# Kernel optimization log

Measured on AMD Instinct MI355X. Metric: run time of the kernel, lower is better.

Reference implementation:

```python
import jax, jax.numpy as jnp
import numpy as np
from jax import lax

# Dense-equivalent of the spconv net: SubMConv/SparseConv with stride 1 and
# size-preserving padding on a dense input reduce to ordinary conv2d.
# Layer chain: (1->64,k1) PReLU (64->256,k3) PReLU (256->512,k3) PReLU
# (512->256,k3) PReLU (256->64,k3) PReLU (64->1,k3) PReLU, then symmetrize.

CHANS = [(1, 64, 1), (64, 256, 3), (256, 512, 3), (512, 256, 3), (256, 64, 3), (64, 1, 3)]


def _conv(x, w, b, k):
    pad = ((k // 2, k // 2), (k // 2, k // 2))
    y = lax.conv_general_dilated(x, w, window_strides=(1, 1), padding=pad,
                                 dimension_numbers=('NCHW', 'OIHW', 'NCHW'))
    return y + b[None, :, None, None]


def _prelu(x, a):
    return jnp.where(x >= 0, x, a * x)


def setup_inputs() -> dict:
    key = jax.random.key(0)
    keys = jax.random.split(key, 1 + 2 * len(CHANS))
    inp = {'A': jax.random.normal(keys[0], (1, 1, 512, 512), dtype=jnp.float32)}
    for i, (cin, cout, k) in enumerate(CHANS):
        fan_in = cin * k * k
        std = 1.0 / np.sqrt(fan_in)
        inp[f'w{i}'] = jax.random.normal(keys[1 + 2 * i], (cout, cin, k, k), dtype=jnp.float32) * std
        inp[f'b{i}'] = jax.random.normal(keys[2 + 2 * i], (cout,), dtype=jnp.float32) * std
        inp[f'p{i}'] = jnp.full((1,), 0.25, dtype=jnp.float32)  # PReLU default weight
    return inp


def reference(A, w0, b0, p0, w1, b1, p1, w2, b2, p2, w3, b3, p3, w4, b4, p4, w5, b5, p5):
    params = [(w0, b0, p0), (w1, b1, p1), (w2, b2, p2), (w3, b3, p3), (w4, b4, p4), (w5, b5, p5)]
    x = A
    for (w, b, p), (_, _, k) in zip(params, CHANS):
        x = _prelu(_conv(x, w, b, k), p)
    # make_symmetric: average with transpose over the spatial (matrix) dims
    return 0.5 * (x + jnp.swapaxes(x, -1, -2))
```

## Files before the change

kernel.cpp:

```cpp
#include <hip/hip_runtime.h>
#include <hip/hip_bf16.h>
#include <stdint.h>

typedef __bf16 bf16_t;
typedef __bf16 bf16x8 __attribute__((ext_vector_type(8)));
typedef float  f32x4  __attribute__((ext_vector_type(4)));

#define HP 514
#define AS1 __attribute__((address_space(1)))
#define AS3 __attribute__((address_space(3)))

__device__ __forceinline__ bf16_t f2bf(float f) { return (bf16_t)f; }

__global__ void l0_kernel(const float* __restrict__ A, const float* __restrict__ w0,
                          const float* __restrict__ b0, const float* __restrict__ p0,
                          bf16_t* __restrict__ X0)
{
    int idx = blockIdx.x * 256 + threadIdx.x;
    if (idx >= HP * HP * 64) return;
    int c   = idx & 63;
    int pix = idx >> 6;
    int py = pix / HP, px = pix - py * HP;
    float v = 0.f;
    if (py >= 1 && py <= 512 && px >= 1 && px <= 512) {
        float a = A[(py - 1) * 512 + (px - 1)];
        v = fmaf(w0[c], a, b0[c]);
        v = v >= 0.f ? v : p0[0] * v;
    }
    X0[idx] = f2bf(v);
}

__global__ void zero_rows_kernel(bf16_t* __restrict__ buf, int C, int r0, int n)
{
    int idx = blockIdx.x * 256 + threadIdx.x;
    int rowsz = HP * C;
    if (idx >= n * rowsz) return;
    int r = idx / rowsz, j = idx - r * rowsz;
    buf[(size_t)(r0 + r) * rowsz + j] = f2bf(0.f);
}

__global__ void zero_cols_kernel(bf16_t* __restrict__ buf, int C, int R)
{
    int idx = blockIdx.x * 256 + threadIdx.x;
    if (idx >= R * 2 * C) return;
    int r = idx / (2 * C);
    int t = idx - r * 2 * C;
    int col = (t < C) ? 0 : 513;
    int c = t % C;
    buf[((size_t)r * HP + col) * C + c] = f2bf(0.f);
}

__global__ void wtrans_kernel(const float* __restrict__ w, bf16_t* __restrict__ wt,
                              int COUT, int CIN)
{
    int idx = blockIdx.x * 256 + threadIdx.x;
    if (idx >= COUT * CIN * 9) return;
    int G    = COUT / 16;
    int j    = idx & 7;
    int l    = (idx >> 3) & 63;
    int t    = idx >> 9;
    int gabs = t % G;
    int t2   = t / G;
    int tap  = t2 % 9;
    int ci   = t2 / 9;
    int cout = gabs * 16 + (l & 15);
    int cin  = ci * 32 + (l >> 4) * 8 + j;
    wt[idx] = f2bf(w[(cout * CIN + cin) * 9 + tap]);
}

template<int CIN, int COUT, int BN>
__global__ __launch_bounds__(256, 3)
void conv3x3_kernel(const bf16_t* __restrict__ in, const bf16_t* __restrict__ wt,
                    const float* __restrict__ bias, const float* __restrict__ alpha,
                    bf16_t* __restrict__ out,
                    int n_rows, int in_off, int in_alloc, int out_off)
{
    constexpr int G      = COUT / 16;
    constexpr int NT     = BN / 32;
    constexpr int NC     = CIN / 32;
    constexpr int AUNITS = 18 * 10 * 4;
    constexpr int APAD   = 768;
    constexpr int ASLAB  = APAD * 8;
    constexpr int ROWB   = BN * 2;
    constexpr int SMASK  = ROWB / 32 - 1;
    constexpr int SMEM_B = (2 * ASLAB * 2 > 128 * ROWB) ? 2 * ASLAB * 2 : 128 * ROWB;
    __shared__ __align__(16) char smem[SMEM_B];
    bf16_t* As = (bf16_t*)smem;

    const int tid  = threadIdx.x;
    const int lane = tid & 63;
    const int wave = tid >> 6;
    const int lm   = lane & 15;
    const int quad = lane >> 4;
    const int wave_m = wave >> 1;
    const int wave_n = wave & 1;

    const int bid  = blockIdx.x + 64 * (blockIdx.y + gridDim.y * blockIdx.z);
    const int nwg  = 64 * gridDim.y * gridDim.z;
    const int sid  = (bid & 7) * (nwg >> 3) + (bid >> 3);
    const int zsh  = __ffs(gridDim.z) - 1;
    const int szb  = sid & (gridDim.z - 1);
    const int t2   = sid >> zsh;
    const int sx   = t2 & 63;
    const int syb  = t2 >> 6;

    const int x0 = sx * 8;
    const int y0 = syb * 16;
    const int zb = szb;
    const int gb_blk = zb * (BN / 16);

    int a_srcb[3];
    #pragma unroll
    for (int it = 0; it < 3; ++it) {
        int u  = it * 256 + tid;
        int uu = u < AUNITS ? u : AUNITS - 1;
        int qq = uu & 3, px = (uu >> 2) % 10, r = uu / 40;
        int q  = (qq - (px >> 1)) & 3;
        int grow = in_off + y0 + r;
        grow = grow < 0 ? 0 : (grow >= in_alloc ? in_alloc - 1 : grow);
        a_srcb[it] = (grow * HP + x0 + px) * CIN + q * 8;
    }

    const int pxb = lm & 7, pyb = lm >> 3;
    int sw[3];
    #pragma unroll
    for (int dx = 0; dx < 3; ++dx)
        sw[dx] = ((quad + ((pxb + dx) >> 1)) & 3) * 8;
    int addrA0[4];
    #pragma unroll
    for (int mt = 0; mt < 4; ++mt)
        addrA0[mt] = ((wave_m * 8 + mt * 2 + pyb) * 40 + pxb * 4) * 8;

    auto stageA = [&](int cc, int abuf) {
        #pragma unroll
        for (int it = 0; it < 3; ++it) {
            const bf16_t* src = in + a_srcb[it] + cc;
            bf16_t* dst = As + abuf * ASLAB + (it * 256 + wave * 64) * 8;
            __builtin_amdgcn_global_load_lds((AS1 void*)src, (AS3 void*)dst, 16, 0, 0);
        }
    };
    auto loadB = [&](int ft, bf16x8* b) {
        const bf16_t* base = wt + ((size_t)ft * G + gb_blk + wave_n * NT) * 512 + lane * 8;
        #pragma unroll
        for (int nt = 0; nt < NT; ++nt)
            b[nt] = *(const bf16x8*)(base + nt * 512);
    };
    auto readA = [&](int ab, int tap, bf16x8* a) {
        const int dy = tap / 3, dx = tap - dy * 3;
        const int shift = (dy * 40 + dx * 4) * 8 + sw[dx];
        #pragma unroll
        for (int mt = 0; mt < 4; ++mt)
            a[mt] = *(const bf16x8*)(As + ab * ASLAB + addrA0[mt] + shift);
    };

    f32x4 acc[4][NT] = {};
    bf16x8 breg[2][NT];
    bf16x8 areg[2][4];

    stageA(0, 0);
    loadB(0, breg[0]);
    __syncthreads();
    readA(0, 0, areg[0]);

    for (int cp = 0; cp < NC / 2; ++cp) {
        const bool morecp = (cp + 1 < NC / 2);
        const int fb = cp * 18;
        #pragma unroll
        for (int rf = 0; rf < 18; ++rf) {
            if (rf < 17 || morecp)
                loadB(fb + rf + 1, breg[(rf + 1) & 1]);
            if (rf == 0)            stageA((2 * cp + 1) * 32, 1);
            if (rf == 9 && morecp)  stageA((2 * cp + 2) * 32, 0);
            if (rf != 8 && rf != 17)
                readA((rf + 1) >= 9 ? 1 : 0, (rf + 1) % 9, areg[(rf + 1) & 1]);

            __builtin_amdgcn_s_setprio(1);
            #pragma unroll
            for (int mt = 0; mt < 4; ++mt)
                #pragma unroll
                for (int nt = 0; nt < NT; ++nt)
                    acc[mt][nt] = __builtin_amdgcn_mfma_f32_16x16x32_bf16(
                        areg[rf & 1][mt], breg[rf & 1][nt], acc[mt][nt], 0, 0, 0);
            __builtin_amdgcn_s_setprio(0);

            if (rf == 8) {
                __syncthreads();
                readA(1, 0, areg[1]);
            }
            if (rf == 17 && morecp) {
                __syncthreads();
                readA(0, 0, areg[0]);
            }
        }
    }

    __syncthreads();
    const float al = alpha[0];
    #pragma unroll
    for (int nt = 0; nt < NT; ++nt) {
        const int c  = wave_n * (BN / 2) + nt * 16 + lm;
        const float bv = bias[zb * BN + c];
        #pragma unroll
        for (int mt = 0; mt < 4; ++mt) {
            f32x4 v = acc[mt][nt];
            #pragma unroll
            for (int r = 0; r < 4; ++r) {
                int m = wave_m * 64 + mt * 16 + quad * 4 + r;
                float f = v[r] + bv;
                f = f >= 0.f ? f : al * f;
                int byte = m * ROWB + ((c * 2) ^ ((m & SMASK) << 5));
                *(bf16_t*)(smem + byte) = f2bf(f);
            }
        }
    }
    __syncthreads();
    constexpr int CPI  = ROWB / 16;
    constexpr int ITER = (128 * CPI) / 256;
    #pragma unroll
    for (int i = 0; i < ITER; ++i) {
        int g = i * 256 + tid;
        int p = g / CPI;
        int k = g & (CPI - 1);
        int sbyte = p * ROWB + ((k * 16) ^ ((p & SMASK) << 5));
        bf16x8 v16 = *(const bf16x8*)(smem + sbyte);
        int py = p >> 3, px = p & 7, ly = y0 + py;
        if (ly < n_rows)
            *(bf16x8*)(out + ((size_t)(out_off + ly) * HP + (x0 + px + 1)) * COUT
                       + zb * BN + k * 8) = v16;
    }
}

__device__ __forceinline__ float conv64_at(const bf16_t* __restrict__ X,
                                           const float* __restrict__ wsh,
                                           int y, int x, float bv)
{
    float acc = bv;
    #pragma unroll
    for (int dy = 0; dy < 3; ++dy) {
        #pragma unroll
        for (int dx = 0; dx < 3; ++dx) {
            const bf16x8* p = (const bf16x8*)(X + ((size_t)(y + dy) * HP + (x + dx)) * 64);
            const float* wf = wsh + (dy * 3 + dx) * 64;
            #pragma unroll
            for (int j = 0; j < 8; ++j) {
                bf16x8 v = p[j];
                #pragma unroll
                for (int k = 0; k < 8; ++k)
                    acc = fmaf((float)v[k], wf[j * 8 + k], acc);
            }
        }
    }
    return acc;
}

__global__ __launch_bounds__(256)
void l5_strip_kernel(const bf16_t* __restrict__ B4, const bf16_t* __restrict__ wt5,
                     const float* __restrict__ b5, const float* __restrict__ p5,
                     float* __restrict__ T, int abs_row0)
{
    __shared__ float wsh[9 * 64];
    for (int i = threadIdx.x; i < 576; i += 256) wsh[i] = (float)wt5[i];
    __syncthreads();
    int idx = blockIdx.x * 256 + threadIdx.x;
    int ly = idx >> 9, x = idx & 511;
    float bv = b5[0], al = p5[0];
    float t = conv64_at(B4, wsh, ly, x, bv);
    t = t >= 0.f ? t : al * t;
    T[(size_t)(abs_row0 + ly) * 512 + x] = t;
}

__global__ void wtrans5_kernel(const float* __restrict__ w, bf16_t* __restrict__ wt)
{
    int idx = blockIdx.x * 256 + threadIdx.x;
    if (idx >= 9 * 64) return;
    int cin = idx % 64, tap = idx / 64;
    wt[idx] = f2bf(w[cin * 9 + tap]);
}

__global__ __launch_bounds__(256)
void sym_kernel(const float* __restrict__ T, float* __restrict__ out)
{
    int idx = blockIdx.x * 256 + threadIdx.x;
    int y = idx >> 9, x = idx & 511;
    out[idx] = 0.5f * (T[idx] + T[x * 512 + y]);
}

extern "C" void kernel_launch(void* const* d_in, const int* in_sizes, int n_in,
                              void* d_out, int out_size, void* d_ws, size_t ws_size,
                              hipStream_t stream)
{
    const float* A = (const float*)d_in[0];
    const float *w[6], *b[6], *p[6];
    for (int i = 0; i < 6; ++i) {
        w[i] = (const float*)d_in[1 + 3 * i];
        b[i] = (const float*)d_in[2 + 3 * i];
        p[i] = (const float*)d_in[3 + 3 * i];
    }

    auto footprint = [](long long S) -> size_t {
        auto al = [](size_t v) { return (v + 255) & ~(size_t)255; };
        size_t t = 0;
        t += al((size_t)HP * HP * 64 * 2);
        t += al((size_t)(S + 8) * HP * 256 * 2);
        t += al((size_t)(S + 6) * HP * 512 * 2);
        t += al((size_t)(S + 2) * HP * 64 * 2);
        t += al((size_t)512 * 512 * 4);
        t += al((size_t)9 * 256 * 64 * 2);
        t += al((size_t)9 * 512 * 256 * 2);
        t += al((size_t)9 * 256 * 512 * 2);
        t += al((size_t)9 * 64 * 256 * 2);
        t += al((size_t)9 * 64 * 2);
        return t;
    };
    const int cand[6] = {512, 256, 128, 64, 32, 16};
    int S = 16;
    for (int i = 0; i < 6; ++i)
        if (footprint(cand[i]) <= ws_size) { S = cand[i]; break; }
    const int nStrips = 512 / S;

    char* ws = (char*)d_ws;
    size_t off = 0;
    auto carve = [&](size_t bytes) -> void* {
        void* r = ws + off;
        off += (bytes + 255) & ~(size_t)255;
        return r;
    };
    bf16_t* X0  = (bf16_t*)carve((size_t)HP * HP * 64 * 2);
    bf16_t* B1  = (bf16_t*)carve((size_t)(S + 8) * HP * 256 * 2);
    bf16_t* B2  = (bf16_t*)carve((size_t)(S + 6) * HP * 512 * 2);
    bf16_t* B4  = (bf16_t*)carve((size_t)(S + 2) * HP * 64 * 2);
    float*  T   = (float*)carve((size_t)512 * 512 * 4);
    bf16_t* wt1 = (bf16_t*)carve((size_t)9 * 256 * 64 * 2);
    bf16_t* wt2 = (bf16_t*)carve((size_t)9 * 512 * 256 * 2);
    bf16_t* wt3 = (bf16_t*)carve((size_t)9 * 256 * 512 * 2);
    bf16_t* wt4 = (bf16_t*)carve((size_t)9 * 64 * 256 * 2);
    bf16_t* wt5 = (bf16_t*)carve((size_t)9 * 64 * 2);
    bf16_t* B3  = B1;

    auto cdiv = [](int a, int bq) { return (a + bq - 1) / bq; };
    auto zrows = [&](bf16_t* buf, int C, int r0, int n) {
        if (n > 0)
            zero_rows_kernel<<<cdiv(n * HP * C, 256), 256, 0, stream>>>(buf, C, r0, n);
    };

    wtrans_kernel<<<cdiv(9 * 256 * 64, 256), 256, 0, stream>>>(w[1], wt1, 256, 64);
    wtrans_kernel<<<cdiv(9 * 512 * 256, 256), 256, 0, stream>>>(w[2], wt2, 512, 256);
    wtrans_kernel<<<cdiv(9 * 256 * 512, 256), 256, 0, stream>>>(w[3], wt3, 256, 512);
    wtrans_kernel<<<cdiv(9 * 64 * 256, 256), 256, 0, stream>>>(w[4], wt4, 64, 256);
    wtrans5_kernel<<<cdiv(9 * 64, 256), 256, 0, stream>>>(w[5], wt5);
    l0_kernel<<<cdiv(HP * HP * 64, 256), 256, 0, stream>>>(A, w[0], b[0], p[0], X0);
    zero_cols_kernel<<<cdiv((S + 8) * 2 * 256, 256), 256, 0, stream>>>(B1, 256, S + 8);
    zero_cols_kernel<<<cdiv((S + 6) * 2 * 512, 256), 256, 0, stream>>>(B2, 512, S + 6);
    zero_cols_kernel<<<cdiv((S + 2) * 2 * 64, 256), 256, 0, stream>>>(B4, 64, S + 2);

    for (int s = 0; s < nStrips; ++s) {
        const int base = S * s;
        int o0[5], nn[5], ooff[5], alloc[5];
        for (int k = 1; k <= 4; ++k) {
            int hk = 5 - k;
            int a0 = base - hk, a1 = base + S + hk;
            int c0 = a0 < 0 ? 0 : a0, c1 = a1 > 512 ? 512 : a1;
            o0[k] = c0; nn[k] = c1 - c0; ooff[k] = c0 - a0; alloc[k] = S + 2 * hk;
        }
        {
            int in_off = o0[1];
            dim3 g(64, cdiv(nn[1], 16), 2);
            conv3x3_kernel<64, 256, 128><<<g, 256, 0, stream>>>(
                X0, wt1, b[1], p[1], B1, nn[1], in_off, 514, ooff[1]);
            zrows(B1, 256, 0, ooff[1]);
            zrows(B1, 256, ooff[1] + nn[1], alloc[1] - ooff[1] - nn[1]);
        }
        {
            int in_off = (o0[2] - 1) - (base - 4);
            dim3 g(64, cdiv(nn[2], 16), 4);
            conv3x3_kernel<256, 512, 128><<<g, 256, 0, stream>>>(
                B1, wt2, b[2], p[2], B2, nn[2], in_off, alloc[1], ooff[2]);
            zrows(B2, 512, 0, ooff[2]);
            zrows(B2, 512, ooff[2] + nn[2], alloc[2] - ooff[2] - nn[2]);
        }
        {
            int in_off = (o0[3] - 1) - (base - 3);
            dim3 g(64, cdiv(nn[3], 16), 2);
            conv3x3_kernel<512, 256, 128><<<g, 256, 0, stream>>>(
                B2, wt3, b[3], p[3], B3, nn[3], in_off, alloc[2], ooff[3]);
            zrows(B3, 256, 0, ooff[3]);
            zrows(B3, 256, ooff[3] + nn[3], alloc[3] - ooff[3] - nn[3]);
        }
        {
            int in_off = (o0[4] - 1) - (base - 2);
            dim3 g(64, cdiv(nn[4], 16), 1);
            conv3x3_kernel<256, 64, 64><<<g, 256, 0, stream>>>(
                B3, wt4, b[4], p[4], B4, nn[4], in_off, alloc[3], ooff[4]);
            zrows(B4, 64, 0, ooff[4]);
            zrows(B4, 64, ooff[4] + nn[4], alloc[4] - ooff[4] - nn[4]);
        }
        l5_strip_kernel<<<(S * 512) / 256, 256, 0, stream>>>(B4, wt5, b[5], p[5], T, base);
    }

    sym_kernel<<<(512 * 512) / 256, 256, 0, stream>>>(T, (float*)d_out);
}
```

Baseline: 1.365 ms.

## Deepen conv3x3 A-tile LDS ring to four slabs and prefetch two chunks ahead

The 3x3 conv kernel's input-tile staging in LDS grows from two slabs to a four-slab ring. Each global_load_lds prefetch is now issued two 32-channel chunks ahead, not one. The first A-fragment read of the next chunk moves ahead of the barrier instead of after it. The aim is to hide more global-load latency behind the MFMA loop and shorten the stall at each barrier. In exchange, LDS use per block roughly doubles for the staging area, which could limit how many blocks fit on a CU.

```diff
diff --git a/kernel.cpp b/kernel.cpp
--- a/kernel.cpp
+++ b/kernel.cpp
@@ -83,7 +83,7 @@
     constexpr int ASLAB  = APAD * 8;
     constexpr int ROWB   = BN * 2;
     constexpr int SMASK  = ROWB / 32 - 1;
-    constexpr int SMEM_B = (2 * ASLAB * 2 > 128 * ROWB) ? 2 * ASLAB * 2 : 128 * ROWB;
+    constexpr int SMEM_B = (4 * ASLAB * 2 > 128 * ROWB) ? 4 * ASLAB * 2 : 128 * ROWB;
     __shared__ __align__(16) char smem[SMEM_B];
     bf16_t* As = (bf16_t*)smem;
 
@@ -131,11 +131,11 @@
     for (int mt = 0; mt < 4; ++mt)
         addrA0[mt] = ((wave_m * 8 + mt * 2 + pyb) * 40 + pxb * 4) * 8;
 
-    auto stageA = [&](int cc, int abuf) {
+    auto stageA = [&](int cc, int base) {
         #pragma unroll
         for (int it = 0; it < 3; ++it) {
             const bf16_t* src = in + a_srcb[it] + cc;
-            bf16_t* dst = As + abuf * ASLAB + (it * 256 + wave * 64) * 8;
+            bf16_t* dst = As + base + (it * 256 + wave * 64) * 8;
             __builtin_amdgcn_global_load_lds((AS1 void*)src, (AS3 void*)dst, 16, 0, 0);
         }
     };
@@ -145,12 +145,12 @@
         for (int nt = 0; nt < NT; ++nt)
             b[nt] = *(const bf16x8*)(base + nt * 512);
     };
-    auto readA = [&](int ab, int tap, bf16x8* a) {
+    auto readA = [&](int base, int tap, bf16x8* a) {
         const int dy = tap / 3, dx = tap - dy * 3;
         const int shift = (dy * 40 + dx * 4) * 8 + sw[dx];
         #pragma unroll
         for (int mt = 0; mt < 4; ++mt)
-            a[mt] = *(const bf16x8*)(As + ab * ASLAB + addrA0[mt] + shift);
+            a[mt] = *(const bf16x8*)(As + base + addrA0[mt] + shift);
     };
 
     f32x4 acc[4][NT] = {};
@@ -158,21 +158,28 @@
     bf16x8 areg[2][4];
 
     stageA(0, 0);
+    stageA(32, ASLAB);
     loadB(0, breg[0]);
     __syncthreads();
     readA(0, 0, areg[0]);
 
     for (int cp = 0; cp < NC / 2; ++cp) {
         const bool morecp = (cp + 1 < NC / 2);
-        const int fb = cp * 18;
+        const int fb  = cp * 18;
+        const int sb0 = ((2 * cp)     & 3) * ASLAB;
+        const int sb1 = ((2 * cp + 1) & 3) * ASLAB;
+        const int sb2 = ((2 * cp + 2) & 3) * ASLAB;
+        const int sb3 = ((2 * cp + 3) & 3) * ASLAB;
         #pragma unroll
         for (int rf = 0; rf < 18; ++rf) {
             if (rf < 17 || morecp)
                 loadB(fb + rf + 1, breg[(rf + 1) & 1]);
-            if (rf == 0)            stageA((2 * cp + 1) * 32, 1);
-            if (rf == 9 && morecp)  stageA((2 * cp + 2) * 32, 0);
-            if (rf != 8 && rf != 17)
-                readA((rf + 1) >= 9 ? 1 : 0, (rf + 1) % 9, areg[(rf + 1) & 1]);
+            if (rf == 0 && 2 * cp + 2 < NC) stageA((2 * cp + 2) * 32, sb2);
+            if (rf == 9 && 2 * cp + 3 < NC) stageA((2 * cp + 3) * 32, sb3);
+            if (rf <= 7)        readA(sb0, rf + 1, areg[(rf + 1) & 1]);
+            else if (rf == 8)   readA(sb1, 0, areg[1]);
+            else if (rf <= 16)  readA(sb1, rf - 8, areg[(rf + 1) & 1]);
+            else if (morecp)    readA(sb2, 0, areg[0]);
 
             __builtin_amdgcn_s_setprio(1);
             #pragma unroll
@@ -183,14 +190,8 @@
                         areg[rf & 1][mt], breg[rf & 1][nt], acc[mt][nt], 0, 0, 0);
             __builtin_amdgcn_s_setprio(0);
 
-            if (rf == 8) {
-                __syncthreads();
-                readA(1, 0, areg[1]);
-            }
-            if (rf == 17 && morecp) {
-                __syncthreads();
-                readA(0, 0, areg[0]);
-            }
+            if (rf == 8)             __syncthreads();
+            if (rf == 17 && morecp)  __syncthreads();
         }
     }
 
```

Measured after the change: 1.384 ms. Within noise of the previous version (+1.4%).
